# Kernel optimization log

Hardware: AMD Instinct MI355X
Metric: run time of the kernel (lower is better)

The kernel has to match this reference:

```python
import jax, jax.numpy as jnp
import numpy as np

NUM_HEADS = 8


def _mab(Q, K, Wq, bq, Wk, bk, Wv, bv, Wo, bo):
    # MAB with ln=False, dropout=0 (eval). Scale is sqrt(dim_V), matching source.
    B, Lq, _ = Q.shape
    Lk = K.shape[1]
    Dv = Wq.shape[1]
    dh = Dv // NUM_HEADS
    q = (Q @ Wq + bq).reshape(B, Lq, NUM_HEADS, dh).transpose(0, 2, 1, 3)
    k = (K @ Wk + bk).reshape(B, Lk, NUM_HEADS, dh).transpose(0, 2, 1, 3)
    v = (K @ Wv + bv).reshape(B, Lk, NUM_HEADS, dh).transpose(0, 2, 1, 3)
    A = jax.nn.softmax(jnp.einsum('bhqd,bhkd->bhqk', q, k) / jnp.sqrt(jnp.float32(Dv)), axis=-1)
    O = (q + jnp.einsum('bhqk,bhkd->bhqd', A, v)).transpose(0, 2, 1, 3).reshape(B, Lq, Dv)
    return O + jax.nn.relu(O @ Wo + bo)


def _forward(x, adj, gin_W, gin_b, geW1, geb1, geW2, geb2,
             gnW1, gnb1, gnW2, gnb2, goW, gob, S,
             mWq, mbq, mWk, mbk, mWv, mbv, mWo, mbo, finW, finb):
    B, V, T, D = x.shape
    Hd = gin_W.shape[1]
    # --- GNN encoder (adj path) ---
    h = x.reshape(B, V, T * D) @ gin_W + gin_b            # [B,V,H]
    # edge_mlp first linear on cat([h_i,h_j]) == h@Wi (row) + h@Wj (col); avoids 2H concat
    Wi, Wj = geW1[:Hd], geW1[Hd:]
    pre = (h @ Wi)[:, :, None, :] + (h @ Wj)[:, None, :, :] + geb1   # [B,V,V,H]
    e = jax.nn.relu(jax.nn.relu(pre) @ geW2 + geb2)       # [B,V,V,H]
    agg = jnp.einsum('bijh,bij->bih', e, adj)             # mask * sum over j, fused
    node = jax.nn.relu(jax.nn.relu(agg @ gnW1 + gnb1) @ gnW2 + gnb2)
    enc = node @ goW + gob                                # [B,V,H]
    # --- decoder: PMA + SAB + SAB + Linear ---
    o = _mab(jnp.broadcast_to(S, (B,) + S.shape[1:]), enc,
             mWq[0], mbq[0], mWk[0], mbk[0], mWv[0], mbv[0], mWo[0], mbo[0])
    o = _mab(o, o, mWq[1], mbq[1], mWk[1], mbk[1], mWv[1], mbv[1], mWo[1], mbo[1])
    o = _mab(o, o, mWq[2], mbq[2], mWk[2], mbk[2], mWv[2], mbv[2], mWo[2], mbo[2])
    out = o @ finW + finb                                 # [B,num_slots,T*OD]
    return out.reshape(B, S.shape[1], T, finW.shape[1] // T)


def setup_inputs() -> dict:
    key = jax.random.key(0)
    ks = jax.random.split(key, 16)
    B, V, T, D = 4, 256, 12, 4
    H, NS, OD = 256, 16, 32

    def w(k, shape, s=0.02):
        return s * jax.random.normal(k, shape, jnp.float32)

    return {
        'x': jax.random.normal(ks[0], (B, V, T, D), jnp.float32),
        'adj': (jax.random.uniform(ks[1], (B, V, V)) > 0.5).astype(jnp.float32),
        'gin_W': w(ks[2], (T * D, H)), 'gin_b': jnp.zeros((H,), jnp.float32),
        'geW1': w(ks[3], (2 * H, H)), 'geb1': jnp.zeros((H,), jnp.float32),
        'geW2': w(ks[4], (H, H)), 'geb2': jnp.zeros((H,), jnp.float32),
        'gnW1': w(ks[5], (H, H)), 'gnb1': jnp.zeros((H,), jnp.float32),
        'gnW2': w(ks[6], (H, H)), 'gnb2': jnp.zeros((H,), jnp.float32),
        'goW': w(ks[7], (H, H)), 'gob': jnp.zeros((H,), jnp.float32),
        'S': w(ks[8], (1, NS, H), 0.05),
        'mWq': w(ks[9], (3, H, H)), 'mbq': jnp.zeros((3, H), jnp.float32),
        'mWk': w(ks[10], (3, H, H)), 'mbk': jnp.zeros((3, H), jnp.float32),
        'mWv': w(ks[11], (3, H, H)), 'mbv': jnp.zeros((3, H), jnp.float32),
        'mWo': w(ks[12], (3, H, H)), 'mbo': jnp.zeros((3, H), jnp.float32),
        'finW': w(ks[13], (H, T * OD)), 'finb': jnp.zeros((T * OD,), jnp.float32),
    }


def reference(x, adj, gin_W, gin_b, geW1, geb1, geW2, geb2,
              gnW1, gnb1, gnW2, gnb2, goW, gob, S,
              mWq, mbq, mWk, mbk, mWv, mbv, mWo, mbo, finW, finb):
    return _forward(x, adj, gin_W, gin_b, geW1, geb1, geW2, geb2,
                    gnW1, gnb1, gnW2, gnb2, goW, gob, S,
                    mWq, mbq, mWk, mbk, mWv, mbv, mWo, mbo, finW, finb)
```

## Files before the change

kernel.cpp:

```cpp
#include <hip/hip_runtime.h>
#include <hip/hip_bf16.h>

typedef unsigned short u16;
typedef __bf16 bf8v __attribute__((ext_vector_type(8)));
typedef float f4v __attribute__((ext_vector_type(4)));

__device__ __forceinline__ float b2f(u16 v) {
  union { unsigned u; float f; } x; x.u = ((unsigned)v) << 16; return x.f;
}
__device__ __forceinline__ u16 f2b(float f) {
  union { float f; unsigned u; } x; x.f = f;
  unsigned r = (x.u + 0x7FFFu + ((x.u >> 16) & 1u)) >> 16;
  return (u16)r;
}
__device__ __forceinline__ unsigned pkbf(float a, float b) {
  union { __hip_bfloat162 h; unsigned u; } c;
  c.h = __float22bfloat162_rn(make_float2(a, b));
  return c.u;
}
__device__ __forceinline__ void up2(unsigned u, float& lo, float& hi) {
  union { unsigned x; float f; } a, b;
  a.x = u << 16; b.x = u & 0xffff0000u; lo = a.f; hi = b.f;
}

#define NFRAG 18

struct PreArgs {
  const float* fsrc[NFRAG];
  u16* fdst[NFRAG];
  int fstride[NFRAG];
  int fbase[NFRAG + 1];
  int fragTiles, hBase, prepBid, q1Bid;
  const float *x, *ginW, *ginb;
  u16* h_bf;
  const float *mbk, *mbv, *mbq, *S, *mWq;
  float *bkv0, *bqkv1, *bqkv2;
  u16* q1b;
  int* bar;
};

__global__ __launch_bounds__(256) void k_pre(PreArgs a) {
  __shared__ __align__(16) char smem[27648];
  const int bid = blockIdx.x, t = threadIdx.x;

  if (bid < a.fragTiles) {
    u16* ld = (u16*)smem;
    int j = 0;
    while (j + 1 < NFRAG && a.fbase[j + 1] <= bid) j++;
    const int localT = bid - a.fbase[j];
    const float* src = a.fsrc[j];
    const int Ns = a.fstride[j];
    const int n0 = localT * 16;
    {
      const float* s = src + (size_t)t * Ns + n0;
      const float4 v0 = ((const float4*)s)[0], v1 = ((const float4*)s)[1];
      const float4 v2 = ((const float4*)s)[2], v3 = ((const float4*)s)[3];
      unsigned* row = (unsigned*)(ld + t * 20);
      row[0] = pkbf(v0.x, v0.y); row[1] = pkbf(v0.z, v0.w);
      row[2] = pkbf(v1.x, v1.y); row[3] = pkbf(v1.z, v1.w);
      row[4] = pkbf(v2.x, v2.y); row[5] = pkbf(v2.z, v2.w);
      row[6] = pkbf(v3.x, v3.y); row[7] = pkbf(v3.z, v3.w);
    }
    __syncthreads();
    u16* dst = a.fdst[j] + (size_t)localT * 4096;
#pragma unroll
    for (int s2 = 0; s2 < 2; s2++) {
      const int o = t * 2 + s2, kt = o >> 6, lane = o & 63;
      const int nlo = lane & 15, bk = kt * 32 + ((lane >> 4) << 3);
      union { u16 h[8]; uint4 q; } pk;
#pragma unroll
      for (int j2 = 0; j2 < 8; j2++) pk.h[j2] = ld[(bk + j2) * 20 + nlo];
      *(uint4*)(dst + (size_t)(kt * 64 + lane) * 8) = pk.q;
    }
    return;
  }
  if (bid < a.prepBid) {
    float (*xs)[48] = (float (*)[48])(smem + 10240);
    const int row0 = (bid - a.hBase) * 4;
    if (t < 192) {
      const int rr = t / 48, k = t % 48;
      xs[rr][k] = a.x[(size_t)(row0 + rr) * 48 + k];
    }
    __syncthreads();
    const float bias = a.ginb[t];
    float acc[4] = {bias, bias, bias, bias};
    for (int k = 0; k < 48; k++) {
      const float w = a.ginW[(size_t)k * 256 + t];
#pragma unroll
      for (int rr = 0; rr < 4; rr++) acc[rr] += xs[rr][k] * w;
    }
#pragma unroll
    for (int rr = 0; rr < 4; rr++) a.h_bf[(size_t)(row0 + rr) * 256 + t] = f2b(acc[rr]);
    return;
  }
  if (bid == a.prepBid) {
    a.bar[t] = 0;
    a.bkv0[t] = a.mbk[t]; a.bkv0[256 + t] = a.mbv[t];
    a.bqkv1[t] = a.mbq[256 + t]; a.bqkv1[256 + t] = a.mbk[256 + t]; a.bqkv1[512 + t] = a.mbv[256 + t];
    a.bqkv2[t] = a.mbq[512 + t]; a.bqkv2[256 + t] = a.mbk[512 + t]; a.bqkv2[512 + t] = a.mbv[512 + t];
    return;
  }
  if (bid == a.q1Bid) {
    float* Ss = (float*)(smem + 11264);
    for (int idx = t; idx < 4096; idx += 256) Ss[idx] = a.S[idx];
    __syncthreads();
    float acc[16];
#pragma unroll
    for (int r = 0; r < 16; r++) acc[r] = 0.f;
    for (int k = 0; k < 256; k++) {
      const float w = a.mWq[(size_t)k * 256 + t];
#pragma unroll
      for (int r = 0; r < 16; r++) acc[r] += Ss[r * 256 + k] * w;
    }
    const float bq = a.mbq[t];
#pragma unroll
    for (int r = 0; r < 16; r++) a.q1b[r * 256 + t] = f2b(acc[r] + bq);
    return;
  }
}

__global__ __launch_bounds__(256) void k_wiwj(
    const u16* __restrict__ h, const u16* __restrict__ frag,
    float* __restrict__ hWiF, u16* __restrict__ hWjB) {
  __shared__ __align__(16) u16 As[64 * 264];
  const int t = threadIdx.x, lane = t & 63, wv = t >> 6;
  const int m0 = blockIdx.x * 64, n0 = blockIdx.y * 128;
  {
    const int row = t >> 2, ch = t & 3;
#pragma unroll
    for (int s = 0; s < 8; s++)
      *(uint4*)(As + row * 264 + ch * 64 + s * 8) =
          *(const uint4*)(h + (size_t)(m0 + row) * 256 + ch * 64 + s * 8);
  }
  __syncthreads();
  f4v acc[4][2];
#pragma unroll
  for (int mt = 0; mt < 4; mt++)
#pragma unroll
    for (int nt = 0; nt < 2; nt++) acc[mt][nt] = (f4v){0.f, 0.f, 0.f, 0.f};
  const int Tw = (n0 >> 4) + wv * 2;
#pragma unroll
  for (int kt = 0; kt < 8; kt++) {
    bf8v af[4], bf[2];
#pragma unroll
    for (int mt = 0; mt < 4; mt++)
      af[mt] = *(const bf8v*)(As + (mt * 16 + (lane & 15)) * 264 + kt * 32 + ((lane >> 4) << 3));
#pragma unroll
    for (int nt = 0; nt < 2; nt++)
      bf[nt] = *(const bf8v*)(frag + ((size_t)((Tw + nt) * 8 + kt) * 64 + lane) * 8);
#pragma unroll
    for (int mt = 0; mt < 4; mt++)
#pragma unroll
      for (int nt = 0; nt < 2; nt++)
        acc[mt][nt] = __builtin_amdgcn_mfma_f32_16x16x32_bf16(af[mt], bf[nt], acc[mt][nt], 0, 0, 0);
  }
#pragma unroll
  for (int mt = 0; mt < 4; mt++)
#pragma unroll
    for (int nt = 0; nt < 2; nt++) {
      const int n = n0 + wv * 32 + nt * 16 + (lane & 15);
      const int mb = m0 + mt * 16 + ((lane >> 4) << 2);
#pragma unroll
      for (int r = 0; r < 4; r++) {
        if (n < 256)
          hWiF[(size_t)(mb + r) * 256 + n] = acc[mt][nt][r];
        else
          hWjB[(size_t)(mb + r) * 256 + (n - 256)] = f2b(acc[mt][nt][r]);
      }
    }
}

__global__ __launch_bounds__(256, 2) void k_edge(
    const float* __restrict__ hWiF, const u16* __restrict__ hWjB,
    const float* __restrict__ adj, const float* __restrict__ geb1,
    const u16* __restrict__ fragW2, const float* __restrict__ geb2,
    u16* __restrict__ aggB) {
  __shared__ __align__(16) u16 As[64 * 280];
  __shared__ float hi[256];
  __shared__ int jlist[256];
  __shared__ int cnt;
  const int t = threadIdx.x, lane = t & 63, wv = t >> 6;
  const int b = blockIdx.x >> 8, i = blockIdx.x & 255;
  if (t == 0) cnt = 0;
  __syncthreads();
  {
    const float a = adj[(size_t)(b * 256 + i) * 256 + t];
    hi[t] = hWiF[(size_t)(b * 256 + i) * 256 + t] + geb1[t];
    if (a != 0.f) { const int p = atomicAdd(&cnt, 1); jlist[p] = t; }
  }
  __syncthreads();
  const int nact = cnt;
  if (nact == 0) {
    if (lane < 16) {
#pragma unroll
      for (int nt = 0; nt < 4; nt++)
        aggB[(size_t)(b * 256 + i) * 256 + wv * 64 + nt * 16 + lane] = 0;
    }
    return;
  }
  const int nch = (nact + 63) >> 6;
  float bias2[4];
#pragma unroll
  for (int nt = 0; nt < 4; nt++) bias2[nt] = geb2[wv * 64 + nt * 16 + (lane & 15)];
  float aggAcc[4] = {0.f, 0.f, 0.f, 0.f};
  const u16* fw = fragW2 + lane * 8;

  for (int c = 0; c < nch; c++) {
    const int rows = min(64, nact - c * 64);
    {
      const int r = t >> 2, q = t & 3;
      const bool valid = (r < rows);
      const int j = valid ? jlist[c * 64 + r] : jlist[0];
      const uint4* s4 = (const uint4*)(hWjB + (size_t)(b * 256 + j) * 256 + q * 64);
      u16* dstrow = As + r * 280 + q * 72;
#pragma unroll
      for (int ii = 0; ii < 8; ii++) {
        const uint4 v = s4[ii];
        const int k = q * 64 + ii * 8;
        float f0, f1, f2, f3, f4, f5, f6, f7;
        up2(v.x, f0, f1); up2(v.y, f2, f3); up2(v.z, f4, f5); up2(v.w, f6, f7);
        uint4 qd;
        qd.x = pkbf(fmaxf(f0 + hi[k + 0], 0.f), fmaxf(f1 + hi[k + 1], 0.f));
        qd.y = pkbf(fmaxf(f2 + hi[k + 2], 0.f), fmaxf(f3 + hi[k + 3], 0.f));
        qd.z = pkbf(fmaxf(f4 + hi[k + 4], 0.f), fmaxf(f5 + hi[k + 5], 0.f));
        qd.w = pkbf(fmaxf(f6 + hi[k + 6], 0.f), fmaxf(f7 + hi[k + 7], 0.f));
        *(uint4*)(dstrow + ii * 8) = qd;
      }
    }
    __syncthreads();
    f4v acc[4][4];
#pragma unroll
    for (int jt = 0; jt < 4; jt++)
#pragma unroll
      for (int nt = 0; nt < 4; nt++) acc[jt][nt] = (f4v){0.f, 0.f, 0.f, 0.f};
    bf8v bcur[4];
#pragma unroll
    for (int nt = 0; nt < 4; nt++)
      bcur[nt] = *(const bf8v*)(fw + (size_t)((wv * 4 + nt) * 8 + 0) * 512);
#pragma unroll
    for (int kt = 0; kt < 8; kt++) {
      bf8v bnxt[4];
      if (kt < 7) {
#pragma unroll
        for (int nt = 0; nt < 4; nt++)
          bnxt[nt] = *(const bf8v*)(fw + (size_t)((wv * 4 + nt) * 8 + kt + 1) * 512);
      }
      bf8v af[4];
      const int coff = (kt >> 1) * 72 + (kt & 1) * 32 + ((lane >> 4) << 3);
#pragma unroll
      for (int jt = 0; jt < 4; jt++)
        af[jt] = *(const bf8v*)(As + (jt * 16 + (lane & 15)) * 280 + coff);
#pragma unroll
      for (int nt = 0; nt < 4; nt++)
#pragma unroll
        for (int jt = 0; jt < 4; jt++)
          acc[jt][nt] = __builtin_amdgcn_mfma_f32_16x16x32_bf16(af[jt], bcur[nt], acc[jt][nt], 0, 0, 0);
      if (kt < 7) {
#pragma unroll
        for (int nt = 0; nt < 4; nt++) bcur[nt] = bnxt[nt];
      }
    }
    const int rbase = (lane >> 4) * 4;
#pragma unroll
    for (int nt = 0; nt < 4; nt++) {
      float s = 0.f;
#pragma unroll
      for (int jt = 0; jt < 4; jt++) {
        const int r0 = jt * 16 + rbase;
#pragma unroll
        for (int r = 0; r < 4; r++) {
          const float e = fmaxf(acc[jt][nt][r] + bias2[nt], 0.f);
          s += (r0 + r < rows) ? e : 0.f;
        }
      }
      s += __shfl_xor(s, 16);
      s += __shfl_xor(s, 32);
      aggAcc[nt] += s;
    }
    __syncthreads();
  }
  if (lane < 16) {
#pragma unroll
    for (int nt = 0; nt < 4; nt++) {
      const int n = wv * 64 + nt * 16 + lane;
      aggB[(size_t)(b * 256 + i) * 256 + n] = f2b(aggAcc[nt]);
    }
  }
}

__device__ __forceinline__ void barArrive(int* c) {
  __syncthreads();
  if (threadIdx.x == 0)
    __hip_atomic_fetch_add(c, 1, __ATOMIC_RELEASE, __HIP_MEMORY_SCOPE_AGENT);
}
__device__ __forceinline__ void barWait(int* c, int target) {
  if (threadIdx.x == 0) {
    int it = 0;
    while (__hip_atomic_load(c, __ATOMIC_ACQUIRE, __HIP_MEMORY_SCOPE_AGENT) < target) {
      __builtin_amdgcn_s_sleep(8);
      if (((++it) & 255) == 0)
        __hip_atomic_fetch_add(c, 0, __ATOMIC_ACQ_REL, __HIP_MEMORY_SCOPE_AGENT);
    }
  }
  __syncthreads();
}

__device__ void g16w(const u16* Al, const u16* __restrict__ frag,
                     const float* bias, int relu, u16* Ol, int t) {
  const int lane = t & 63, w = t >> 6;
  f4v acc = (f4v){0.f, 0.f, 0.f, 0.f};
  const u16* abase = Al + (lane & 15) * 264 + ((lane >> 4) << 3);
  const u16* fb = frag + ((size_t)(w * 8) * 64 + lane) * 8;
  bf8v bc = *(const bf8v*)fb;
#pragma unroll
  for (int kt = 0; kt < 8; kt++) {
    bf8v bn;
    if (kt < 7) bn = *(const bf8v*)(fb + (size_t)(kt + 1) * 512);
    const bf8v af = *(const bf8v*)(abase + kt * 32);
    acc = __builtin_amdgcn_mfma_f32_16x16x32_bf16(af, bc, acc, 0, 0, 0);
    if (kt < 7) bc = bn;
  }
  const int col = w * 16 + (lane & 15);
  const float bv = bias[col];
#pragma unroll
  for (int r = 0; r < 4; r++) {
    const int row = ((lane >> 4) << 2) + r;
    float v = acc[r] + bv;
    if (relu) v = fmaxf(v, 0.f);
    Ol[row * 264 + col] = f2b(v);
  }
}

__device__ void g16kv2(const u16* Al, const u16* __restrict__ frag,
                       const float* bias, u16* outG, int t) {
  const int lane = t & 63, w = t >> 6;
  f4v acc[2];
  acc[0] = (f4v){0.f, 0.f, 0.f, 0.f};
  acc[1] = (f4v){0.f, 0.f, 0.f, 0.f};
  const u16* abase = Al + (lane & 15) * 264 + ((lane >> 4) << 3);
  const u16* f0 = frag + ((size_t)((w * 2 + 0) * 8) * 64 + lane) * 8;
  const u16* f1 = frag + ((size_t)((w * 2 + 1) * 8) * 64 + lane) * 8;
  bf8v bc0 = *(const bf8v*)f0;
  bf8v bc1 = *(const bf8v*)f1;
#pragma unroll
  for (int kt = 0; kt < 8; kt++) {
    bf8v bn0, bn1;
    if (kt < 7) {
      bn0 = *(const bf8v*)(f0 + (size_t)(kt + 1) * 512);
      bn1 = *(const bf8v*)(f1 + (size_t)(kt + 1) * 512);
    }
    const bf8v af = *(const bf8v*)(abase + kt * 32);
    acc[0] = __builtin_amdgcn_mfma_f32_16x16x32_bf16(af, bc0, acc[0], 0, 0, 0);
    acc[1] = __builtin_amdgcn_mfma_f32_16x16x32_bf16(af, bc1, acc[1], 0, 0, 0);
    if (kt < 7) { bc0 = bn0; bc1 = bn1; }
  }
#pragma unroll
  for (int nt = 0; nt < 2; nt++) {
    const int col = (w * 2 + nt) * 16 + (lane & 15);
    const float bv = bias[col];
#pragma unroll
    for (int r = 0; r < 4; r++) {
      const int row = ((lane >> 4) << 2) + r;
      outG[(size_t)row * 512 + col] = f2b(acc[nt][r] + bv);
    }
  }
}

__device__ void attn_half(const u16* __restrict__ qbuf,
                          const u16* __restrict__ kbuf, const u16* __restrict__ vbuf,
                          float* __restrict__ oF, u16* __restrict__ oB,
                          int b, int hd, int half, float* qs, float* sc, float* vs, int t) {
  const int lane = t & 63, w = t >> 6;
  const int Lk = 256;
  if (t < 64) {
    const int row = t >> 2, part = t & 3;
    const uint4 q4 = *(const uint4*)(qbuf + (size_t)row * 256 + hd * 32 + part * 8);
    float f0, f1, f2, f3, f4, f5, f6, f7;
    up2(q4.x, f0, f1); up2(q4.y, f2, f3); up2(q4.z, f4, f5); up2(q4.w, f6, f7);
    float4* d = (float4*)(qs + row * 32 + part * 8);
    d[0] = make_float4(f0, f1, f2, f3);
    d[1] = make_float4(f4, f5, f6, f7);
  }
  __syncthreads();
  if (t < 256) {
    float kv[32];
    const uint4* kp = (const uint4*)(kbuf + (size_t)(b * Lk + t) * 512 + hd * 32);
#pragma unroll
    for (int c4 = 0; c4 < 4; c4++) {
      const uint4 k4 = kp[c4];
      up2(k4.x, kv[c4 * 8 + 0], kv[c4 * 8 + 1]);
      up2(k4.y, kv[c4 * 8 + 2], kv[c4 * 8 + 3]);
      up2(k4.z, kv[c4 * 8 + 4], kv[c4 * 8 + 5]);
      up2(k4.w, kv[c4 * 8 + 6], kv[c4 * 8 + 7]);
    }
    for (int r = 0; r < 8; r++) {
      const int grow = half * 8 + r;
      float s = 0.f;
#pragma unroll
      for (int d = 0; d < 32; d++) s += qs[grow * 32 + d] * kv[d];
      sc[r * 256 + t] = s * 0.0625f;
    }
  }
  __syncthreads();
  if (w < 8) {
    const int r = w;
    float v[4];
    float mx = -1e30f;
#pragma unroll
    for (int q2 = 0; q2 < 4; q2++) {
      v[q2] = sc[r * 256 + lane + q2 * 64];
      mx = fmaxf(mx, v[q2]);
    }
    for (int off = 32; off; off >>= 1) mx = fmaxf(mx, __shfl_xor(mx, off));
    float sum = 0.f;
#pragma unroll
    for (int q2 = 0; q2 < 4; q2++) { v[q2] = __expf(v[q2] - mx); sum += v[q2]; }
    for (int off = 32; off; off >>= 1) sum += __shfl_xor(sum, off);
    const float inv = 1.f / sum;
#pragma unroll
    for (int q2 = 0; q2 < 4; q2++) sc[r * 256 + lane + q2 * 64] = v[q2] * inv;
  }
  __syncthreads();
  {
    const int row = t >> 2, part = t & 3;
    const uint4 v4 = *(const uint4*)(vbuf + (size_t)(b * Lk + row) * 512 + hd * 32 + part * 8);
    float f0, f1, f2, f3, f4, f5, f6, f7;
    up2(v4.x, f0, f1); up2(v4.y, f2, f3); up2(v4.z, f4, f5); up2(v4.w, f6, f7);
    float4* d = (float4*)(vs + row * 32 + part * 8);
    d[0] = make_float4(f0, f1, f2, f3);
    d[1] = make_float4(f4, f5, f6, f7);
  }
  __syncthreads();
  if (t < 256) {
    const int r0 = t >> 5, d = t & 31;
    const int grow = half * 8 + r0;
    float a0 = qs[grow * 32 + d];
#pragma unroll 4
    for (int j = 0; j < Lk; j++) a0 += sc[r0 * 256 + j] * vs[j * 32 + d];
    const int c0 = hd * 32 + d;
    oF[(size_t)(b * 16 + grow) * 256 + c0] = a0;
    oB[(size_t)(b * 16 + grow) * 256 + c0] = f2b(a0);
  }
}

__device__ void wprojG(const u16* __restrict__ o1b, const float* __restrict__ o1f,
                       const u16* __restrict__ frag, const float* __restrict__ bias,
                       u16* actL, float* residL, int b, int T, int lane) {
  f4v acc = (f4v){0.f, 0.f, 0.f, 0.f};
  const u16* abase = o1b + (size_t)(b * 16 + (lane & 15)) * 256 + ((lane >> 4) << 3);
  const u16* fbase = frag + ((size_t)(T * 8) * 64 + lane) * 8;
#pragma unroll
  for (int kt = 0; kt < 8; kt++)
    acc = __builtin_amdgcn_mfma_f32_16x16x32_bf16(*(const bf8v*)(abase + kt * 32),
                                                  *(const bf8v*)(fbase + (size_t)kt * 512), acc, 0, 0, 0);
  const int col = T * 16 + (lane & 15);
  const float bv = bias[col];
#pragma unroll
  for (int r = 0; r < 4; r++) {
    const int row = ((lane >> 4) << 2) + r;
    const float v = fmaxf(acc[r] + bv, 0.f) + o1f[(size_t)(b * 16 + row) * 256 + col];
    residL[row * 256 + col] = v;
    actL[row * 264 + col] = f2b(v);
  }
}

template <int NT>
__device__ __forceinline__ void wprojQn(
    const u16* actL, const u16* __restrict__ frag,
    const float* __restrict__ bias, u16* qkvL, int T0, int lane) {
  f4v acc[NT];
#pragma unroll
  for (int nt = 0; nt < NT; nt++) acc[nt] = (f4v){0.f, 0.f, 0.f, 0.f};
  const u16* abase = actL + (lane & 15) * 264 + ((lane >> 4) << 3);
#pragma unroll
  for (int kt = 0; kt < 8; kt++) {
    const bf8v af = *(const bf8v*)(abase + kt * 32);
#pragma unroll
    for (int nt = 0; nt < NT; nt++) {
      const bf8v bf = *(const bf8v*)(frag + ((size_t)((T0 + nt) * 8 + kt) * 64 + lane) * 8);
      acc[nt] = __builtin_amdgcn_mfma_f32_16x16x32_bf16(af, bf, acc[nt], 0, 0, 0);
    }
  }
#pragma unroll
  for (int nt = 0; nt < NT; nt++) {
    const int col = (T0 + nt) * 16 + (lane & 15);
    const float bv = bias[col];
#pragma unroll
    for (int r = 0; r < 4; r++) {
      const int row = ((lane >> 4) << 2) + r;
      qkvL[row * 776 + col] = f2b(acc[nt][r] + bv);
    }
  }
}

__device__ void wprojR(const u16* actIn, const u16* __restrict__ frag,
                       const float* __restrict__ bias, u16* actOut, float* residL,
                       int T, int lane) {
  f4v acc = (f4v){0.f, 0.f, 0.f, 0.f};
  const u16* abase = actIn + (lane & 15) * 264 + ((lane >> 4) << 3);
  const u16* fbase = frag + ((size_t)(T * 8) * 64 + lane) * 8;
#pragma unroll
  for (int kt = 0; kt < 8; kt++)
    acc = __builtin_amdgcn_mfma_f32_16x16x32_bf16(*(const bf8v*)(abase + kt * 32),
                                                  *(const bf8v*)(fbase + (size_t)kt * 512), acc, 0, 0, 0);
  const int col = T * 16 + (lane & 15);
  const float bv = bias[col];
#pragma unroll
  for (int r = 0; r < 4; r++) {
    const int row = ((lane >> 4) << 2) + r;
    const float v = fmaxf(acc[r] + bv, 0.f) + residL[row * 256 + col];
    residL[row * 256 + col] = v;
    actOut[row * 264 + col] = f2b(v);
  }
}

__device__ void wprojF(const u16* actL, const u16* __restrict__ frag,
                       const float* __restrict__ bias, float* __restrict__ outG,
                       int T, int lane) {
  f4v acc = (f4v){0.f, 0.f, 0.f, 0.f};
  const u16* abase = actL + (lane & 15) * 264 + ((lane >> 4) << 3);
  const u16* fbase = frag + ((size_t)(T * 8) * 64 + lane) * 8;
#pragma unroll
  for (int kt = 0; kt < 8; kt++)
    acc = __builtin_amdgcn_mfma_f32_16x16x32_bf16(*(const bf8v*)(abase + kt * 32),
                                                  *(const bf8v*)(fbase + (size_t)kt * 512), acc, 0, 0, 0);
  const int col = T * 16 + (lane & 15);
  const float bv = bias[col];
#pragma unroll
  for (int r = 0; r < 4; r++) {
    const int row = ((lane >> 4) << 2) + r;
    outG[(size_t)row * 384 + col] = acc[r] + bv;
  }
}

__device__ void attnB(const u16* qkvL, float* residL, u16* actOut, float* ps,
                      int hd, int lane) {
  const int r = lane & 15, cg = lane >> 4;
  float qv[32];
  {
    const uint4* qp = (const uint4*)(qkvL + r * 776 + hd * 32);
#pragma unroll
    for (int c4 = 0; c4 < 4; c4++) {
      const uint4 q4 = qp[c4];
      up2(q4.x, qv[c4 * 8 + 0], qv[c4 * 8 + 1]);
      up2(q4.y, qv[c4 * 8 + 2], qv[c4 * 8 + 3]);
      up2(q4.z, qv[c4 * 8 + 4], qv[c4 * 8 + 5]);
      up2(q4.w, qv[c4 * 8 + 6], qv[c4 * 8 + 7]);
    }
  }
  float p[4];
#pragma unroll
  for (int c = 0; c < 4; c++) {
    const int cc = cg * 4 + c;
    const uint4* kp = (const uint4*)(qkvL + cc * 776 + 256 + hd * 32);
    float s = 0.f;
#pragma unroll
    for (int c4 = 0; c4 < 4; c4++) {
      const uint4 k4 = kp[c4];
      float k0, k1;
      up2(k4.x, k0, k1); s += qv[c4 * 8 + 0] * k0 + qv[c4 * 8 + 1] * k1;
      up2(k4.y, k0, k1); s += qv[c4 * 8 + 2] * k0 + qv[c4 * 8 + 3] * k1;
      up2(k4.z, k0, k1); s += qv[c4 * 8 + 4] * k0 + qv[c4 * 8 + 5] * k1;
      up2(k4.w, k0, k1); s += qv[c4 * 8 + 6] * k0 + qv[c4 * 8 + 7] * k1;
    }
    p[c] = s * 0.0625f;
  }
  float mx = fmaxf(fmaxf(p[0], p[1]), fmaxf(p[2], p[3]));
  mx = fmaxf(mx, __shfl_xor(mx, 16));
  mx = fmaxf(mx, __shfl_xor(mx, 32));
  float sum = 0.f;
#pragma unroll
  for (int c = 0; c < 4; c++) { p[c] = __expf(p[c] - mx); sum += p[c]; }
  sum += __shfl_xor(sum, 16);
  sum += __shfl_xor(sum, 32);
  const float inv = 1.f / sum;
#pragma unroll
  for (int c = 0; c < 4; c++) ps[r * 16 + cg * 4 + c] = p[c] * inv;
  float o[8];
#pragma unroll
  for (int j = 0; j < 8; j++) o[j] = qv[cg * 8 + j];
#pragma unroll
  for (int c = 0; c < 16; c++) {
    const float pv = ps[r * 16 + c];
    const uint4 v4 = *(const uint4*)(qkvL + c * 776 + 512 + hd * 32 + cg * 8);
    float v0, v1;
    up2(v4.x, v0, v1); o[0] += pv * v0; o[1] += pv * v1;
    up2(v4.y, v0, v1); o[2] += pv * v0; o[3] += pv * v1;
    up2(v4.z, v0, v1); o[4] += pv * v0; o[5] += pv * v1;
    up2(v4.w, v0, v1); o[6] += pv * v0; o[7] += pv * v1;
  }
  const int col0 = hd * 32 + cg * 8;
#pragma unroll
  for (int j = 0; j < 8; j++) residL[r * 256 + col0 + j] = o[j];
  unsigned* ob = (unsigned*)(actOut + r * 264 + col0);
  ob[0] = pkbf(o[0], o[1]); ob[1] = pkbf(o[2], o[3]);
  ob[2] = pkbf(o[4], o[5]); ob[3] = pkbf(o[6], o[7]);
}

struct TailArgs {
  const u16 *agg, *fGn1, *fGn2, *fGo, *fKV0, *fQKV1, *fQKV2, *fO0, *fO1, *fO2, *fFin, *q1b;
  const float *gnb1, *gnb2, *gob, *bkv0, *bqkv1, *bqkv2, *mbo, *finb;
  u16 *kv1, *o1b;
  float *o1f, *outF;
  int* bar;
};

__global__ __launch_bounds__(1024) void k_tailM(TailArgs a) {
  __shared__ __align__(16) char smem[58112];
  const int bid = blockIdx.x, t = threadIdx.x;
  const int lane = t & 63, w = t >> 6;
  const int g = bid >> 4, m = bid & 15;
  int* c1 = a.bar + g * 32;
  int* c2 = a.bar + g * 32 + 16;

  {
    u16* actA = (u16*)smem;
    u16* actB = (u16*)(smem + 8448);
    const int r0 = bid * 16;
    if (t < 512) {
      const int row = t >> 5, ch = t & 31;
      *(uint4*)(actA + row * 264 + ch * 8) =
          *(const uint4*)(a.agg + (size_t)(r0 + row) * 256 + ch * 8);
    }
    __syncthreads();
    g16w(actA, a.fGn1, a.gnb1, 1, actB, t); __syncthreads();
    g16w(actB, a.fGn2, a.gnb2, 1, actA, t); __syncthreads();
    g16w(actA, a.fGo, a.gob, 0, actB, t); __syncthreads();
    g16kv2(actB, a.fKV0, a.bkv0, a.kv1 + (size_t)r0 * 512, t);
  }
  barArrive(c1);
  barWait(c1, 16);
  {
    float* qs = (float*)smem;
    float* sc = (float*)(smem + 2048);
    float* vs = (float*)(smem + 18432);
    attn_half(a.q1b, a.kv1, a.kv1 + 256, a.o1f, a.o1b,
              g, m & 7, m >> 3, qs, sc, vs, t);
  }
  barArrive(c2);
  if (m != 0) return;
  barWait(c2, 16);
  {
    const int b = g;
    u16* act0 = (u16*)smem;
    u16* act1 = (u16*)(smem + 8448);
    u16* qkvL = (u16*)(smem + 16896);
    float* residL = (float*)(smem + 41728);
    float* psL = (float*)smem;
    wprojG(a.o1b, a.o1f, a.fO0, a.mbo, act0, residL, b, w, lane);
    __syncthreads();
    wprojQn<3>(act0, a.fQKV1, a.bqkv1, qkvL, w * 3, lane);
    __syncthreads();
    if (w < 8) attnB(qkvL, residL, act1, psL + w * 256, w, lane);
    __syncthreads();
    wprojR(act1, a.fO1, a.mbo + 256, act0, residL, w, lane);
    __syncthreads();
    wprojQn<3>(act0, a.fQKV2, a.bqkv2, qkvL, w * 3, lane);
    __syncthreads();
    if (w < 8) attnB(qkvL, residL, act1, psL + w * 256, w, lane);
    __syncthreads();
    wprojR(act1, a.fO2, a.mbo + 512, act0, residL, w, lane);
    __syncthreads();
    for (int T = w; T < 24; T += 16)
      wprojF(act0, a.fFin, a.finb, a.outF + (size_t)b * 16 * 384, T, lane);
  }
}

extern "C" void kernel_launch(void* const* d_in, const int* in_sizes, int n_in,
                              void* d_out, int out_size, void* d_ws, size_t ws_size,
                              hipStream_t stream) {
  const float* x    = (const float*)d_in[0];
  const float* adj  = (const float*)d_in[1];
  const float* ginW = (const float*)d_in[2];
  const float* ginb = (const float*)d_in[3];
  const float* geW1 = (const float*)d_in[4];
  const float* geb1 = (const float*)d_in[5];
  const float* geW2 = (const float*)d_in[6];
  const float* geb2 = (const float*)d_in[7];
  const float* gnW1 = (const float*)d_in[8];
  const float* gnb1 = (const float*)d_in[9];
  const float* gnW2 = (const float*)d_in[10];
  const float* gnb2 = (const float*)d_in[11];
  const float* goW  = (const float*)d_in[12];
  const float* gob  = (const float*)d_in[13];
  const float* S    = (const float*)d_in[14];
  const float* mWq  = (const float*)d_in[15];
  const float* mbq  = (const float*)d_in[16];
  const float* mWk  = (const float*)d_in[17];
  const float* mbk  = (const float*)d_in[18];
  const float* mWv  = (const float*)d_in[19];
  const float* mbv  = (const float*)d_in[20];
  const float* mWo  = (const float*)d_in[21];
  const float* mbo  = (const float*)d_in[22];
  const float* finW = (const float*)d_in[23];
  const float* finb = (const float*)d_in[24];
  (void)in_sizes; (void)n_in; (void)out_size; (void)ws_size;

  char* wp = (char*)d_ws;
  size_t off = 0;
  auto alloc = [&](size_t bytes) -> char* {
    char* p = wp + off;
    off += (bytes + 255) & ~(size_t)255;
    return p;
  };
  u16* h_bf     = (u16*)alloc(1024 * 256 * 2);
  float* hWiF   = (float*)alloc((size_t)1024 * 256 * 4);
  u16* hWjB     = (u16*)alloc(1024 * 256 * 2);
  u16* fWiWj    = (u16*)alloc(512 * 256 * 2);
  u16* fW2      = (u16*)alloc(256 * 256 * 2);
  u16* fGn1     = (u16*)alloc(256 * 256 * 2);
  u16* fGn2     = (u16*)alloc(256 * 256 * 2);
  u16* fGo      = (u16*)alloc(256 * 256 * 2);
  u16* fKV0     = (u16*)alloc(512 * 256 * 2);
  u16* fQKV1    = (u16*)alloc(768 * 256 * 2);
  u16* fQKV2    = (u16*)alloc(768 * 256 * 2);
  u16* fO0      = (u16*)alloc(256 * 256 * 2);
  u16* fO1      = (u16*)alloc(256 * 256 * 2);
  u16* fO2      = (u16*)alloc(256 * 256 * 2);
  u16* fFin     = (u16*)alloc(384 * 256 * 2);
  float* bkv0   = (float*)alloc(512 * 4);
  float* bqkv1  = (float*)alloc(768 * 4);
  float* bqkv2  = (float*)alloc(768 * 4);
  u16* q1b      = (u16*)alloc(16 * 256 * 2);
  u16* agg_b    = (u16*)alloc(1024 * 256 * 2);
  u16* kv1      = (u16*)alloc(1024 * 512 * 2);
  float* o1f    = (float*)alloc(64 * 256 * 4);
  u16* o1b      = (u16*)alloc(64 * 256 * 2);
  int* bar      = (int*)alloc(1024);

  PreArgs P{};
  int nj = 0, tiles = 0;
  auto addF = [&](const float* s, int stride, u16* d, int nT) {
    P.fsrc[nj] = s; P.fdst[nj] = d; P.fstride[nj] = stride; P.fbase[nj] = tiles;
    tiles += nT; nj++;
  };
  addF(geW1, 256, fWiWj, 16);
  addF(geW1 + 65536, 256, fWiWj + 16 * 4096, 16);
  addF(geW2, 256, fW2, 16);
  addF(gnW1, 256, fGn1, 16);
  addF(gnW2, 256, fGn2, 16);
  addF(goW, 256, fGo, 16);
  addF(mWk, 256, fKV0, 16);
  addF(mWv, 256, fKV0 + 16 * 4096, 16);
  addF(mWq + 65536, 256, fQKV1, 16);
  addF(mWk + 65536, 256, fQKV1 + 16 * 4096, 16);
  addF(mWv + 65536, 256, fQKV1 + 32 * 4096, 16);
  addF(mWq + 131072, 256, fQKV2, 16);
  addF(mWk + 131072, 256, fQKV2 + 16 * 4096, 16);
  addF(mWv + 131072, 256, fQKV2 + 32 * 4096, 16);
  addF(mWo, 256, fO0, 16);
  addF(mWo + 65536, 256, fO1, 16);
  addF(mWo + 131072, 256, fO2, 16);
  addF(finW, 384, fFin, 24);
  P.fbase[nj] = tiles;
  P.fragTiles = tiles;
  P.hBase = tiles;
  P.prepBid = tiles + 256;
  P.q1Bid = tiles + 257;
  P.x = x; P.ginW = ginW; P.ginb = ginb; P.h_bf = h_bf;
  P.mbk = mbk; P.mbv = mbv; P.mbq = mbq; P.S = S; P.mWq = mWq;
  P.bkv0 = bkv0; P.bqkv1 = bqkv1; P.bqkv2 = bqkv2; P.q1b = q1b;
  P.bar = bar;

  TailArgs T{};
  T.agg = agg_b; T.fGn1 = fGn1; T.fGn2 = fGn2; T.fGo = fGo; T.fKV0 = fKV0;
  T.fQKV1 = fQKV1; T.fQKV2 = fQKV2; T.fO0 = fO0; T.fO1 = fO1; T.fO2 = fO2;
  T.fFin = fFin; T.q1b = q1b;
  T.gnb1 = gnb1; T.gnb2 = gnb2; T.gob = gob;
  T.bkv0 = bkv0; T.bqkv1 = bqkv1; T.bqkv2 = bqkv2; T.mbo = mbo; T.finb = finb;
  T.kv1 = kv1; T.o1b = o1b; T.o1f = o1f; T.outF = (float*)d_out;
  T.bar = bar;

  k_pre<<<dim3(tiles + 258), dim3(256), 0, stream>>>(P);
  k_wiwj<<<dim3(16, 4), dim3(256), 0, stream>>>(h_bf, fWiWj, hWiF, hWjB);
  k_edge<<<dim3(1024), dim3(256), 0, stream>>>(hWiF, hWjB, adj, geb1, fW2, geb2, agg_b);
  k_tailM<<<dim3(64), dim3(1024), 0, stream>>>(T);
}
```

Measured before the change: 218.7 us.

## Split decoder SAB stages across four blocks per batch with global barriers

The two SAB layers and the final linear used to run in a single block per batch, with all intermediates held in LDS. They now run across four blocks per batch. Activations, QKV and the residual move to global scratch buffers, and a new inter-block atomic barrier (p3bar) is placed between each stage. The aim is to spread the tail GEMM and attention work over more CUs. In exchange the stages pay seven global barrier round trips and extra global-memory traffic where they previously used only cheap __syncthreads.

```diff
diff --git a/kernel.cpp b/kernel.cpp
--- a/kernel.cpp
+++ b/kernel.cpp
@@ -304,6 +304,19 @@
   }
   __syncthreads();
 }
+__device__ __forceinline__ void p3bar(int* c, int target) {
+  __syncthreads();
+  if (threadIdx.x == 0) {
+    __hip_atomic_fetch_add(c, 1, __ATOMIC_RELEASE, __HIP_MEMORY_SCOPE_AGENT);
+    int it = 0;
+    while (__hip_atomic_load(c, __ATOMIC_ACQUIRE, __HIP_MEMORY_SCOPE_AGENT) < target) {
+      __builtin_amdgcn_s_sleep(8);
+      if (((++it) & 255) == 0)
+        __hip_atomic_fetch_add(c, 0, __ATOMIC_ACQ_REL, __HIP_MEMORY_SCOPE_AGENT);
+    }
+  }
+  __syncthreads();
+}
 
 __device__ void g16w(const u16* Al, const u16* __restrict__ frag,
                      const float* bias, int relu, u16* Ol, int t) {
@@ -443,9 +456,9 @@
   }
 }
 
-__device__ void wprojG(const u16* __restrict__ o1b, const float* __restrict__ o1f,
-                       const u16* __restrict__ frag, const float* __restrict__ bias,
-                       u16* actL, float* residL, int b, int T, int lane) {
+__device__ void wprojG_g(const u16* __restrict__ o1b, const float* __restrict__ o1f,
+                         const u16* __restrict__ frag, const float* __restrict__ bias,
+                         u16* act, float* resid, int b, int T, int lane) {
   f4v acc = (f4v){0.f, 0.f, 0.f, 0.f};
   const u16* abase = o1b + (size_t)(b * 16 + (lane & 15)) * 256 + ((lane >> 4) << 3);
   const u16* fbase = frag + ((size_t)(T * 8) * 64 + lane) * 8;
@@ -459,45 +472,15 @@
   for (int r = 0; r < 4; r++) {
     const int row = ((lane >> 4) << 2) + r;
     const float v = fmaxf(acc[r] + bv, 0.f) + o1f[(size_t)(b * 16 + row) * 256 + col];
-    residL[row * 256 + col] = v;
-    actL[row * 264 + col] = f2b(v);
-  }
-}
-
-template <int NT>
-__device__ __forceinline__ void wprojQn(
-    const u16* actL, const u16* __restrict__ frag,
-    const float* __restrict__ bias, u16* qkvL, int T0, int lane) {
-  f4v acc[NT];
-#pragma unroll
-  for (int nt = 0; nt < NT; nt++) acc[nt] = (f4v){0.f, 0.f, 0.f, 0.f};
-  const u16* abase = actL + (lane & 15) * 264 + ((lane >> 4) << 3);
-#pragma unroll
-  for (int kt = 0; kt < 8; kt++) {
-    const bf8v af = *(const bf8v*)(abase + kt * 32);
-#pragma unroll
-    for (int nt = 0; nt < NT; nt++) {
-      const bf8v bf = *(const bf8v*)(frag + ((size_t)((T0 + nt) * 8 + kt) * 64 + lane) * 8);
-      acc[nt] = __builtin_amdgcn_mfma_f32_16x16x32_bf16(af, bf, acc[nt], 0, 0, 0);
-    }
-  }
-#pragma unroll
-  for (int nt = 0; nt < NT; nt++) {
-    const int col = (T0 + nt) * 16 + (lane & 15);
-    const float bv = bias[col];
-#pragma unroll
-    for (int r = 0; r < 4; r++) {
-      const int row = ((lane >> 4) << 2) + r;
-      qkvL[row * 776 + col] = f2b(acc[nt][r] + bv);
-    }
-  }
-}
-
-__device__ void wprojR(const u16* actIn, const u16* __restrict__ frag,
-                       const float* __restrict__ bias, u16* actOut, float* residL,
-                       int T, int lane) {
+    resid[(size_t)(b * 16 + row) * 256 + col] = v;
+    act[(size_t)(b * 16 + row) * 256 + col] = f2b(v);
+  }
+}
+
+__device__ void wprojQ_g(const u16* __restrict__ act, const u16* __restrict__ frag,
+                         const float* __restrict__ bias, u16* qkv, int b, int T, int lane) {
   f4v acc = (f4v){0.f, 0.f, 0.f, 0.f};
-  const u16* abase = actIn + (lane & 15) * 264 + ((lane >> 4) << 3);
+  const u16* abase = act + (size_t)(b * 16 + (lane & 15)) * 256 + ((lane >> 4) << 3);
   const u16* fbase = frag + ((size_t)(T * 8) * 64 + lane) * 8;
 #pragma unroll
   for (int kt = 0; kt < 8; kt++)
@@ -508,17 +491,15 @@
 #pragma unroll
   for (int r = 0; r < 4; r++) {
     const int row = ((lane >> 4) << 2) + r;
-    const float v = fmaxf(acc[r] + bv, 0.f) + residL[row * 256 + col];
-    residL[row * 256 + col] = v;
-    actOut[row * 264 + col] = f2b(v);
-  }
-}
-
-__device__ void wprojF(const u16* actL, const u16* __restrict__ frag,
-                       const float* __restrict__ bias, float* __restrict__ outG,
-                       int T, int lane) {
+    qkv[(size_t)(b * 16 + row) * 768 + col] = f2b(acc[r] + bv);
+  }
+}
+
+__device__ void wprojR_g(const u16* __restrict__ actIn, const u16* __restrict__ frag,
+                         const float* __restrict__ bias, u16* actOut, float* resid,
+                         int b, int T, int lane) {
   f4v acc = (f4v){0.f, 0.f, 0.f, 0.f};
-  const u16* abase = actL + (lane & 15) * 264 + ((lane >> 4) << 3);
+  const u16* abase = actIn + (size_t)(b * 16 + (lane & 15)) * 256 + ((lane >> 4) << 3);
   const u16* fbase = frag + ((size_t)(T * 8) * 64 + lane) * 8;
 #pragma unroll
   for (int kt = 0; kt < 8; kt++)
@@ -529,16 +510,37 @@
 #pragma unroll
   for (int r = 0; r < 4; r++) {
     const int row = ((lane >> 4) << 2) + r;
-    outG[(size_t)row * 384 + col] = acc[r] + bv;
-  }
-}
-
-__device__ void attnB(const u16* qkvL, float* residL, u16* actOut, float* ps,
-                      int hd, int lane) {
+    const float v = fmaxf(acc[r] + bv, 0.f) + resid[(size_t)(b * 16 + row) * 256 + col];
+    resid[(size_t)(b * 16 + row) * 256 + col] = v;
+    actOut[(size_t)(b * 16 + row) * 256 + col] = f2b(v);
+  }
+}
+
+__device__ void wprojF_g(const u16* __restrict__ act, const u16* __restrict__ frag,
+                         const float* __restrict__ bias, float* __restrict__ outF,
+                         int b, int T, int lane) {
+  f4v acc = (f4v){0.f, 0.f, 0.f, 0.f};
+  const u16* abase = act + (size_t)(b * 16 + (lane & 15)) * 256 + ((lane >> 4) << 3);
+  const u16* fbase = frag + ((size_t)(T * 8) * 64 + lane) * 8;
+#pragma unroll
+  for (int kt = 0; kt < 8; kt++)
+    acc = __builtin_amdgcn_mfma_f32_16x16x32_bf16(*(const bf8v*)(abase + kt * 32),
+                                                  *(const bf8v*)(fbase + (size_t)kt * 512), acc, 0, 0, 0);
+  const int col = T * 16 + (lane & 15);
+  const float bv = bias[col];
+#pragma unroll
+  for (int r = 0; r < 4; r++) {
+    const int row = ((lane >> 4) << 2) + r;
+    outF[(size_t)(b * 16 + row) * 384 + col] = acc[r] + bv;
+  }
+}
+
+__device__ void attnB_g(const u16* __restrict__ qkv, float* resid, u16* actOut,
+                        float* ps, int b, int hd, int lane) {
   const int r = lane & 15, cg = lane >> 4;
   float qv[32];
   {
-    const uint4* qp = (const uint4*)(qkvL + r * 776 + hd * 32);
+    const uint4* qp = (const uint4*)(qkv + (size_t)(b * 16 + r) * 768 + hd * 32);
 #pragma unroll
     for (int c4 = 0; c4 < 4; c4++) {
       const uint4 q4 = qp[c4];
@@ -552,7 +554,7 @@
 #pragma unroll
   for (int c = 0; c < 4; c++) {
     const int cc = cg * 4 + c;
-    const uint4* kp = (const uint4*)(qkvL + cc * 776 + 256 + hd * 32);
+    const uint4* kp = (const uint4*)(qkv + (size_t)(b * 16 + cc) * 768 + 256 + hd * 32);
     float s = 0.f;
 #pragma unroll
     for (int c4 = 0; c4 < 4; c4++) {
@@ -582,7 +584,7 @@
 #pragma unroll
   for (int c = 0; c < 16; c++) {
     const float pv = ps[r * 16 + c];
-    const uint4 v4 = *(const uint4*)(qkvL + c * 776 + 512 + hd * 32 + cg * 8);
+    const uint4 v4 = *(const uint4*)(qkv + (size_t)(b * 16 + c) * 768 + 512 + hd * 32 + cg * 8);
     float v0, v1;
     up2(v4.x, v0, v1); o[0] += pv * v0; o[1] += pv * v1;
     up2(v4.y, v0, v1); o[2] += pv * v0; o[3] += pv * v1;
@@ -591,8 +593,8 @@
   }
   const int col0 = hd * 32 + cg * 8;
 #pragma unroll
-  for (int j = 0; j < 8; j++) residL[r * 256 + col0 + j] = o[j];
-  unsigned* ob = (unsigned*)(actOut + r * 264 + col0);
+  for (int j = 0; j < 8; j++) resid[(size_t)(b * 16 + r) * 256 + col0 + j] = o[j];
+  unsigned* ob = (unsigned*)(actOut + (size_t)(b * 16 + r) * 256 + col0);
   ob[0] = pkbf(o[0], o[1]); ob[1] = pkbf(o[2], o[3]);
   ob[2] = pkbf(o[4], o[5]); ob[3] = pkbf(o[6], o[7]);
 }
@@ -602,16 +604,19 @@
   const float *gnb1, *gnb2, *gob, *bkv0, *bqkv1, *bqkv2, *mbo, *finb;
   u16 *kv1, *o1b;
   float *o1f, *outF;
+  u16 *act0, *act1, *qkv;
+  float* resid;
   int* bar;
 };
 
 __global__ __launch_bounds__(1024) void k_tailM(TailArgs a) {
-  __shared__ __align__(16) char smem[58112];
+  __shared__ __align__(16) char smem[58368];
   const int bid = blockIdx.x, t = threadIdx.x;
   const int lane = t & 63, w = t >> 6;
   const int g = bid >> 4, m = bid & 15;
-  int* c1 = a.bar + g * 32;
-  int* c2 = a.bar + g * 32 + 16;
+  int* c1 = a.bar + g * 64;
+  int* c2 = a.bar + g * 64 + 16;
+  int* c3 = a.bar + g * 64 + 32;
 
   {
     u16* actA = (u16*)smem;
@@ -638,31 +643,26 @@
               g, m & 7, m >> 3, qs, sc, vs, t);
   }
   barArrive(c2);
-  if (m != 0) return;
+  if (m >= 4) return;
   barWait(c2, 16);
   {
     const int b = g;
-    u16* act0 = (u16*)smem;
-    u16* act1 = (u16*)(smem + 8448);
-    u16* qkvL = (u16*)(smem + 16896);
-    float* residL = (float*)(smem + 41728);
-    float* psL = (float*)smem;
-    wprojG(a.o1b, a.o1f, a.fO0, a.mbo, act0, residL, b, w, lane);
-    __syncthreads();
-    wprojQn<3>(act0, a.fQKV1, a.bqkv1, qkvL, w * 3, lane);
-    __syncthreads();
-    if (w < 8) attnB(qkvL, residL, act1, psL + w * 256, w, lane);
-    __syncthreads();
-    wprojR(act1, a.fO1, a.mbo + 256, act0, residL, w, lane);
-    __syncthreads();
-    wprojQn<3>(act0, a.fQKV2, a.bqkv2, qkvL, w * 3, lane);
-    __syncthreads();
-    if (w < 8) attnB(qkvL, residL, act1, psL + w * 256, w, lane);
-    __syncthreads();
-    wprojR(act1, a.fO2, a.mbo + 512, act0, residL, w, lane);
-    __syncthreads();
-    for (int T = w; T < 24; T += 16)
-      wprojF(act0, a.fFin, a.finb, a.outF + (size_t)b * 16 * 384, T, lane);
+    float* psW = (float*)smem + w * 256;
+    if (w < 4)  wprojG_g(a.o1b, a.o1f, a.fO0, a.mbo, a.act0, a.resid, b, m * 4 + w, lane);
+    p3bar(c3, 4 * 1);
+    if (w < 12) wprojQ_g(a.act0, a.fQKV1, a.bqkv1, a.qkv, b, m * 12 + w, lane);
+    p3bar(c3, 4 * 2);
+    if (w < 2)  attnB_g(a.qkv, a.resid, a.act1, psW, b, m * 2 + w, lane);
+    p3bar(c3, 4 * 3);
+    if (w < 4)  wprojR_g(a.act1, a.fO1, a.mbo + 256, a.act0, a.resid, b, m * 4 + w, lane);
+    p3bar(c3, 4 * 4);
+    if (w < 12) wprojQ_g(a.act0, a.fQKV2, a.bqkv2, a.qkv, b, m * 12 + w, lane);
+    p3bar(c3, 4 * 5);
+    if (w < 2)  attnB_g(a.qkv, a.resid, a.act1, psW, b, m * 2 + w, lane);
+    p3bar(c3, 4 * 6);
+    if (w < 4)  wprojR_g(a.act1, a.fO2, a.mbo + 512, a.act0, a.resid, b, m * 4 + w, lane);
+    p3bar(c3, 4 * 7);
+    if (w < 6)  wprojF_g(a.act0, a.fFin, a.finb, a.outF, b, m * 6 + w, lane);
   }
 }
 
@@ -726,6 +726,10 @@
   u16* kv1      = (u16*)alloc(1024 * 512 * 2);
   float* o1f    = (float*)alloc(64 * 256 * 4);
   u16* o1b      = (u16*)alloc(64 * 256 * 2);
+  u16* act0_g   = (u16*)alloc(64 * 256 * 2);
+  u16* act1_g   = (u16*)alloc(64 * 256 * 2);
+  u16* qkv_g    = (u16*)alloc(64 * 768 * 2);
+  float* resid_g= (float*)alloc(64 * 256 * 4);
   int* bar      = (int*)alloc(1024);
 
   PreArgs P{};
@@ -769,6 +773,7 @@
   T.gnb1 = gnb1; T.gnb2 = gnb2; T.gob = gob;
   T.bkv0 = bkv0; T.bqkv1 = bqkv1; T.bqkv2 = bqkv2; T.mbo = mbo; T.finb = finb;
   T.kv1 = kv1; T.o1b = o1b; T.o1f = o1f; T.outF = (float*)d_out;
+  T.act0 = act0_g; T.act1 = act1_g; T.qkv = qkv_g; T.resid = resid_g;
   T.bar = bar;
 
   k_pre<<<dim3(tiles + 258), dim3(256), 0, stream>>>(P);
```

Result: no change. 218.6 us (-0.0%).
